# Optimization experiments

Measured on AMD Instinct MI355X. Metric: run time of the kernel, lower is better.

Reference implementation:

```python
import jax, jax.numpy as jnp
import numpy as np

B, T, D_MODEL = 2, 1024, 512
EXPAND = 2
D_INNER = D_MODEL * EXPAND
STATE = 16
K_CONV = 4


def setup_inputs() -> dict:
    key = jax.random.key(0)
    ks = jax.random.split(key, 10)
    sc = lambda k, shape: jax.random.normal(k, shape, jnp.float32) * 0.02
    return {
        "x": jax.random.normal(ks[0], (B, T, D_MODEL), jnp.float32),
        "ln_g": jnp.ones((D_MODEL,), jnp.float32),
        "ln_b": jnp.zeros((D_MODEL,), jnp.float32),
        "W_in": sc(ks[1], (2 * D_INNER, D_MODEL)),
        "conv_w": sc(ks[2], (D_INNER, 1, K_CONV)),
        "conv_b": jnp.zeros((D_INNER,), jnp.float32),
        "W_B": sc(ks[3], (STATE, D_INNER)),
        "W_C": sc(ks[4], (STATE, D_INNER)),
        "W_dt": sc(ks[5], (D_INNER, D_INNER)),
        "b_dt": jax.random.uniform(ks[6], (D_INNER,), jnp.float32, -4.0, -1.0),
        # log_A init: A_diag = -(n+1) from HiPPO, log(-A_diag) = log(n+1), broadcast over d_inner
        "log_A": jnp.broadcast_to(jnp.log(jnp.arange(1, STATE + 1, dtype=jnp.float32)), (D_INNER, STATE)),
        "W_out": sc(ks[7], (D_MODEL, D_INNER)),
    }


def _silu(v):
    return v * jax.nn.sigmoid(v)


def reference(x, ln_g, ln_b, W_in, conv_w, conv_b, W_B, W_C, W_dt, b_dt, log_A, W_out):
    residual = x
    # LayerNorm (biased variance, eps=1e-5)
    mu = x.mean(-1, keepdims=True)
    var = x.var(-1, keepdims=True)
    xn = (x - mu) * jax.lax.rsqrt(var + 1e-5) * ln_g + ln_b
    # input projection and gate split
    xz = xn @ W_in.T                      # (B,T,2*D_INNER)
    x_main, z = jnp.split(xz, 2, axis=-1)
    # depthwise causal conv1d (padding=3 then slice to T == left-pad 3)
    xc = jnp.transpose(x_main, (0, 2, 1))  # (B,D_INNER,T)
    xc = jax.lax.conv_general_dilated(
        xc, conv_w, window_strides=(1,), padding=[(K_CONV - 1, 0)],
        dimension_numbers=("NCH", "OIH", "NCH"), feature_group_count=D_INNER,
    ) + conv_b[None, :, None]
    x_main = _silu(jnp.transpose(xc, (0, 2, 1)))  # (B,T,D_INNER)
    # selective scan in fp32
    xf = x_main.astype(jnp.float32)
    Bt = xf @ W_B.T                        # (B,T,N)
    Ct = xf @ W_C.T                        # (B,T,N)
    dt = jax.nn.softplus(xf @ W_dt.T + b_dt)  # (B,T,D_INNER)
    A = -jnp.exp(log_A)                    # (D_INNER,N)
    dA = jnp.exp(A[None, None] * dt[..., None])              # (B,T,D_INNER,N)
    dBx = dt[..., None] * Bt[:, :, None, :] * xf[..., None]  # (B,T,D_INNER,N)

    def comb(c1, c2):
        a1, b1 = c1
        a2, b2 = c2
        return a1 * a2, a2 * b1 + b2

    _, h = jax.lax.associative_scan(comb, (dA, dBx), axis=1)  # h_t = dA_t*h_{t-1}+dBx_t
    y = (h * Ct[:, :, None, :]).sum(-1).astype(x.dtype)       # (B,T,D_INNER)
    out = (y * _silu(z)) @ W_out.T
    return residual + out
```

## Files before the change

### kernel.cpp

```cpp
#include <hip/hip_runtime.h>

#define T_SEQ 1024
#define DM 512
#define DI 1024
#define NS 16
#define NC 64
#define CL 16

typedef __attribute__((ext_vector_type(8))) short short8;
typedef __attribute__((ext_vector_type(4))) float f32x4;
typedef unsigned short u16;
typedef unsigned int u32;

__device__ inline float b2f(u16 u) {
    unsigned v = ((unsigned)u) << 16;
    return __builtin_bit_cast(float, v);
}
__device__ inline u16 f2b(float f) {
    unsigned u = __builtin_bit_cast(unsigned, f);
    u += 0x7fff + ((u >> 16) & 1);
    return (u16)(u >> 16);
}

__device__ inline void g2l16(const u16* g, short* l) {
    __builtin_amdgcn_global_load_lds((const __attribute__((address_space(1))) u32*)g,
                                     (__attribute__((address_space(3))) u32*)l, 16, 0, 0);
}

__global__ __launch_bounds__(256) void prep_k(const float* __restrict__ Win, const float* __restrict__ Wdt,
                       const float* __restrict__ Wout, const float* __restrict__ Wb,
                       const float* __restrict__ Wc,
                       u16* __restrict__ oWin, u16* __restrict__ oWdt, u16* __restrict__ oWout,
                       u16* __restrict__ oWb, u16* __restrict__ oWc,
                       const float* __restrict__ x, const float* __restrict__ g,
                       const float* __restrict__ be, u16* __restrict__ xn) {
    if (blockIdx.x < 2592) {
        int i = blockIdx.x * 256 + threadIdx.x;
        const float* s; u16* d; int off;
        if (i < 262144)      { s = Win;  d = oWin;  off = i; }
        else if (i < 524288) { s = Wdt;  d = oWdt;  off = i - 262144; }
        else if (i < 655360) { s = Wout; d = oWout; off = i - 524288; }
        else if (i < 659456) { s = Wb;   d = oWb;   off = i - 655360; }
        else                 { s = Wc;   d = oWc;   off = i - 659456; }
        float4 v = ((const float4*)s)[off];
        d[off * 4 + 0] = f2b(v.x);
        d[off * 4 + 1] = f2b(v.y);
        d[off * 4 + 2] = f2b(v.z);
        d[off * 4 + 3] = f2b(v.w);
        return;
    }
    int row = blockIdx.x - 2592, tid = threadIdx.x;
    float2 v = ((const float2*)(x + row * DM))[tid];
    float s = v.x + v.y, q = v.x * v.x + v.y * v.y;
    #pragma unroll
    for (int m = 1; m < 64; m <<= 1) { s += __shfl_xor(s, m); q += __shfl_xor(q, m); }
    __shared__ float ss[4], qq[4];
    if ((tid & 63) == 0) { ss[tid >> 6] = s; qq[tid >> 6] = q; }
    __syncthreads();
    s = ss[0] + ss[1] + ss[2] + ss[3];
    q = qq[0] + qq[1] + qq[2] + qq[3];
    float mu = s / DM;
    float var = q / DM - mu * mu;
    float rs = rsqrtf(var + 1e-5f);
    int c = tid * 2;
    xn[row * DM + c]     = f2b((v.x - mu) * rs * g[c] + be[c]);
    xn[row * DM + c + 1] = f2b((v.y - mu) * rs * g[c + 1] + be[c + 1]);
}

template<int BM, int BN, int NT, int EPI>
__global__ __launch_bounds__(256) void gemm_bt(const u16* __restrict__ A, int lda,
                                               const u16* __restrict__ Bw, int ldb,
                                               void* __restrict__ outp, int ldo,
                                               const float* __restrict__ extra) {
    __shared__ short a_sh[2][BM * 64];
    __shared__ short b_sh[2][BN * 64];
    constexpr int MI = BM / 32, NJ = BN / 32;
    int tid = threadIdx.x, w = tid >> 6, lane = tid & 63;
    int m0 = blockIdx.x * BM, n0 = blockIdx.y * BN;
    int wr = (w >> 1) * (BM / 2), wc = (w & 1) * (BN / 2);
    int lr = lane & 15, kg = lane >> 4;
    f32x4 acc[MI][NJ] = {};
    const u16* Abase = A + (size_t)m0 * lda;
    const u16* Bbase = Bw + (size_t)n0 * ldb;
    int lrow = lane >> 3;
    int lchunk = lane & 7;
    int schunk = lchunk ^ lrow;

    auto stage = [&](int cur, int kt) {
        int k0 = kt * 64;
        #pragma unroll
        for (int r = 0; r < BM / 32; ++r) {
            int row = r * 32 + w * 8 + lrow;
            g2l16(Abase + (size_t)row * lda + k0 + schunk * 8,
                  &a_sh[cur][(r * 32 + w * 8) * 64 + lane * 8]);
        }
        #pragma unroll
        for (int r = 0; r < BN / 32; ++r) {
            int row = r * 32 + w * 8 + lrow;
            g2l16(Bbase + (size_t)row * ldb + k0 + schunk * 8,
                  &b_sh[cur][(r * 32 + w * 8) * 64 + lane * 8]);
        }
    };

    stage(0, 0);
    __syncthreads();
    int cur = 0;
    for (int t = 0; t < NT; ++t) {
        if (t + 1 < NT) stage(cur ^ 1, t + 1);
        #pragma unroll
        for (int kk = 0; kk < 2; ++kk) {
            short8 af[MI], bfr[NJ];
            #pragma unroll
            for (int i = 0; i < MI; ++i) {
                int row = wr + i * 16 + lr;
                af[i] = *(const short8*)&a_sh[cur][row * 64 + (((kk << 2) | kg) ^ (row & 7)) * 8];
            }
            #pragma unroll
            for (int j = 0; j < NJ; ++j) {
                int row = wc + j * 16 + lr;
                bfr[j] = *(const short8*)&b_sh[cur][row * 64 + (((kk << 2) | kg) ^ (row & 7)) * 8];
            }
            #pragma unroll
            for (int i = 0; i < MI; ++i)
                #pragma unroll
                for (int j = 0; j < NJ; ++j)
                    acc[i][j] = __builtin_amdgcn_mfma_f32_16x16x32_bf16(af[i], bfr[j], acc[i][j], 0, 0, 0);
        }
        __syncthreads();
        cur ^= 1;
    }

    int rb = (lane >> 4) * 4, cc = lane & 15;
    #pragma unroll
    for (int i = 0; i < MI; ++i) {
        #pragma unroll
        for (int j = 0; j < NJ; ++j) {
            #pragma unroll
            for (int r = 0; r < 4; ++r) {
                int row = m0 + wr + i * 16 + rb + r;
                int col = n0 + wc + j * 16 + cc;
                float v = acc[i][j][r];
                if (EPI == 0) {
                    ((u16*)outp)[(size_t)row * ldo + col] = f2b(v);
                } else if (EPI == 1) {
                    float xx = v + extra[col];
                    float sp = (xx > 20.f) ? xx : log1pf(__expf(xx));
                    ((u16*)outp)[(size_t)row * ldo + col] = f2b(sp);
                } else {
                    ((float*)outp)[(size_t)row * ldo + col] = v + extra[(size_t)row * ldo + col];
                }
            }
        }
    }
}

__global__ void conv_k(const u16* __restrict__ xz, const float* __restrict__ w,
                       const float* __restrict__ cb, u16* __restrict__ xf) {
    int idx = blockIdx.x * 256 + threadIdx.x;
    int d = idx & (DI - 1);
    int bt = idx >> 10;
    int t = bt & (T_SEQ - 1);
    float s = cb[d];
    #pragma unroll
    for (int i = 0; i < 4; ++i) {
        int tt = t - 3 + i;
        if (tt >= 0) s += w[d * 4 + i] * b2f(xz[(size_t)(bt - 3 + i) * 2048 + d]);
    }
    float sig = 1.f / (1.f + __expf(-s));
    xf[idx] = f2b(s * sig);
}

__global__ __launch_bounds__(256) void bc_k(const u16* __restrict__ xf, const u16* __restrict__ Wb,
                                            const u16* __restrict__ Wc,
                                            float* __restrict__ Bt, float* __restrict__ Ct) {
    int m = blockIdx.x * 8 + (threadIdx.x >> 5);
    int j = threadIdx.x & 31;
    const u16* wrow = (j < 16) ? (Wb + j * DI) : (Wc + (j - 16) * DI);
    const short8* xr = (const short8*)(xf + (size_t)m * DI);
    const short8* wr = (const short8*)wrow;
    float s = 0.f;
    #pragma unroll 4
    for (int k = 0; k < DI / 8; ++k) {
        short8 a = xr[k], b = wr[k];
        #pragma unroll
        for (int e = 0; e < 8; ++e) s += b2f((u16)a[e]) * b2f((u16)b[e]);
    }
    float* o = (j < 16) ? Bt : Ct;
    o[(size_t)m * NS + (j & 15)] = s;
}

__global__ __launch_bounds__(256) void scanA(const u16* __restrict__ dt, const u16* __restrict__ xf,
                                             const float* __restrict__ Bt, const float* __restrict__ logA,
                                             float* __restrict__ Aprod, float* __restrict__ S) {
    int tid = threadIdx.x;
    int dblk = blockIdx.x & 3;
    int c = (blockIdx.x >> 2) & (NC - 1);
    int b = blockIdx.x >> 8;
    int d = dblk * 256 + tid;
    float Adn[NS], ap[NS], h[NS];
    #pragma unroll
    for (int j = 0; j < 4; ++j)
        *(float4*)&Adn[j * 4] = ((const float4*)(logA + (size_t)d * NS))[j];
    #pragma unroll
    for (int n = 0; n < NS; ++n) { Adn[n] = -__expf(Adn[n]); ap[n] = 1.f; h[n] = 0.f; }
    const u16* dtp = dt + ((size_t)b * T_SEQ + c * CL) * DI + d;
    const u16* xfp = xf + ((size_t)b * T_SEQ + c * CL) * DI + d;
    const float* Bp = Bt + ((size_t)b * T_SEQ + c * CL) * NS;
    #pragma unroll
    for (int i = 0; i < CL; ++i) {
        float dtv = b2f(dtp[(size_t)i * DI]);
        float xv  = b2f(xfp[(size_t)i * DI]);
        float ux = dtv * xv;
        float Bv[NS];
        #pragma unroll
        for (int j = 0; j < 4; ++j) *(float4*)&Bv[j * 4] = ((const float4*)(Bp + (size_t)i * NS))[j];
        #pragma unroll
        for (int n = 0; n < NS; ++n) {
            float dA = __expf(Adn[n] * dtv);
            h[n] = fmaf(dA, h[n], ux * Bv[n]);
            ap[n] *= dA;
        }
    }
    size_t o = ((((size_t)c * 2 + b) * DI) + d) * NS;
    #pragma unroll
    for (int j = 0; j < 4; ++j) {
        ((float4*)(Aprod + o))[j] = *(float4*)&ap[j * 4];
        ((float4*)(S + o))[j]     = *(float4*)&h[j * 4];
    }
}

__global__ __launch_bounds__(256) void scanB(const float* __restrict__ Aprod, const float* __restrict__ S,
                                             float* __restrict__ Hin) {
    int chain = blockIdx.x * 256 + threadIdx.x;
    float h = 0.f;
    #pragma unroll 8
    for (int c = 0; c < NC; ++c) {
        size_t o = (size_t)c * 32768 + chain;
        Hin[o] = h;
        h = fmaf(Aprod[o], h, S[o]);
    }
}

__global__ __launch_bounds__(256) void scanC(const u16* __restrict__ dt, const u16* __restrict__ xf,
                                             const float* __restrict__ Bt, const float* __restrict__ Ct,
                                             const float* __restrict__ logA, const float* __restrict__ Hin,
                                             const u16* __restrict__ xz, u16* __restrict__ ym) {
    int tid = threadIdx.x;
    int dblk = blockIdx.x & 3;
    int c = (blockIdx.x >> 2) & (NC - 1);
    int b = blockIdx.x >> 8;
    int d = dblk * 256 + tid;
    float Adn[NS], h[NS];
    #pragma unroll
    for (int j = 0; j < 4; ++j)
        *(float4*)&Adn[j * 4] = ((const float4*)(logA + (size_t)d * NS))[j];
    #pragma unroll
    for (int n = 0; n < NS; ++n) Adn[n] = -__expf(Adn[n]);
    size_t o = ((((size_t)c * 2 + b) * DI) + d) * NS;
    #pragma unroll
    for (int j = 0; j < 4; ++j) *(float4*)&h[j * 4] = ((const float4*)(Hin + o))[j];
    const u16* dtp = dt + ((size_t)b * T_SEQ + c * CL) * DI + d;
    const u16* xfp = xf + ((size_t)b * T_SEQ + c * CL) * DI + d;
    const float* Bp = Bt + ((size_t)b * T_SEQ + c * CL) * NS;
    const float* Cp = Ct + ((size_t)b * T_SEQ + c * CL) * NS;
    const u16* zp = xz + ((size_t)b * T_SEQ + c * CL) * 2048 + 1024 + d;
    u16* yp = ym + ((size_t)b * T_SEQ + c * CL) * DI + d;
    #pragma unroll
    for (int i = 0; i < CL; ++i) {
        float dtv = b2f(dtp[(size_t)i * DI]);
        float xv  = b2f(xfp[(size_t)i * DI]);
        float ux = dtv * xv;
        float Bv[NS], Cv[NS];
        #pragma unroll
        for (int j = 0; j < 4; ++j) {
            *(float4*)&Bv[j * 4] = ((const float4*)(Bp + (size_t)i * NS))[j];
            *(float4*)&Cv[j * 4] = ((const float4*)(Cp + (size_t)i * NS))[j];
        }
        float r = 0.f;
        #pragma unroll
        for (int n = 0; n < NS; ++n) {
            float dA = __expf(Adn[n] * dtv);
            h[n] = fmaf(dA, h[n], ux * Bv[n]);
            r = fmaf(h[n], Cv[n], r);
        }
        float zv = b2f(zp[(size_t)i * 2048]);
        float sz = zv / (1.f + __expf(-zv));
        yp[(size_t)i * DI] = f2b(r * sz);
    }
}

extern "C" void kernel_launch(void* const* d_in, const int* in_sizes, int n_in,
                              void* d_out, int out_size, void* d_ws, size_t ws_size,
                              hipStream_t stream) {
    const float* x     = (const float*)d_in[0];
    const float* ln_g  = (const float*)d_in[1];
    const float* ln_b  = (const float*)d_in[2];
    const float* W_in  = (const float*)d_in[3];
    const float* conv_w= (const float*)d_in[4];
    const float* conv_b= (const float*)d_in[5];
    const float* W_B   = (const float*)d_in[6];
    const float* W_C   = (const float*)d_in[7];
    const float* W_dt  = (const float*)d_in[8];
    const float* b_dt  = (const float*)d_in[9];
    const float* log_A = (const float*)d_in[10];
    const float* W_out = (const float*)d_in[11];

    char* ws = (char*)d_ws;
    u16* wInB  = (u16*)(ws + 0);
    u16* wDtB  = (u16*)(ws + 2097152);
    u16* wOutB = (u16*)(ws + 4194304);
    u16* wBB   = (u16*)(ws + 5242880);
    u16* wCB   = (u16*)(ws + 5275648);
    u16* xnB   = (u16*)(ws + 5308416);
    u16* xzB   = (u16*)(ws + 7405568);
    u16* xfB   = (u16*)(ws + 15794176);
    u16* dtB   = (u16*)(ws + 19988480);
    float* BtF = (float*)(ws + 24182784);
    float* CtF = (float*)(ws + 24313856);
    u16* ymB   = (u16*)(ws + 24444928);
    float* ApF = (float*)(ws + 28639232);
    float* SF  = (float*)(ws + 37027840);
    float* HiF = (float*)(ws + 45416448);

    prep_k<<<4640, 256, 0, stream>>>(W_in, W_dt, W_out, W_B, W_C, wInB, wDtB, wOutB, wBB, wCB,
                                     x, ln_g, ln_b, xnB);
    gemm_bt<64, 64, 8, 0><<<dim3(32, 32), 256, 0, stream>>>(xnB, 512, wInB, 512, (void*)xzB, 2048, nullptr);
    conv_k<<<8192, 256, 0, stream>>>(xzB, conv_w, conv_b, xfB);
    gemm_bt<64, 64, 16, 1><<<dim3(32, 16), 256, 0, stream>>>(xfB, 1024, wDtB, 1024, (void*)dtB, 1024, b_dt);
    bc_k<<<256, 256, 0, stream>>>(xfB, wBB, wCB, BtF, CtF);
    scanA<<<512, 256, 0, stream>>>(dtB, xfB, BtF, log_A, ApF, SF);
    scanB<<<128, 256, 0, stream>>>(ApF, SF, HiF);
    scanC<<<512, 256, 0, stream>>>(dtB, xfB, BtF, CtF, log_A, HiF, xzB, ymB);
    gemm_bt<32, 64, 16, 2><<<dim3(64, 8), 256, 0, stream>>>(ymB, 1024, wOutB, 1024, d_out, 512, x);
}
```

Baseline: 126.7 us.

## Fuse B/C projections into dt GEMM, triple-buffer GEMM loads, halve scan chunks

```diff
diff --git a/kernel.cpp b/kernel.cpp
--- a/kernel.cpp
+++ b/kernel.cpp
@@ -4,8 +4,8 @@
 #define DM 512
 #define DI 1024
 #define NS 16
-#define NC 64
-#define CL 16
+#define NC 32
+#define CL 32
 
 typedef __attribute__((ext_vector_type(8))) short short8;
 typedef __attribute__((ext_vector_type(4))) float f32x4;
@@ -22,26 +22,36 @@
     return (u16)(u >> 16);
 }
 
-__device__ inline void g2l16(const u16* g, short* l) {
+__device__ inline void g2l16(const u16* g, const short* l) {
     __builtin_amdgcn_global_load_lds((const __attribute__((address_space(1))) u32*)g,
                                      (__attribute__((address_space(3))) u32*)l, 16, 0, 0);
+}
+
+template<int K> __device__ __forceinline__ void vmwait() {
+    if constexpr (K == 0) asm volatile("s_waitcnt vmcnt(0)" ::: "memory");
+    else if constexpr (K == 3) asm volatile("s_waitcnt vmcnt(3)" ::: "memory");
+    else if constexpr (K == 4) asm volatile("s_waitcnt vmcnt(4)" ::: "memory");
 }
 
 __global__ __launch_bounds__(256) void prep_k(const float* __restrict__ Win, const float* __restrict__ Wdt,
                        const float* __restrict__ Wout, const float* __restrict__ Wb,
                        const float* __restrict__ Wc,
-                       u16* __restrict__ oWin, u16* __restrict__ oWdt, u16* __restrict__ oWout,
-                       u16* __restrict__ oWb, u16* __restrict__ oWc,
+                       u16* __restrict__ oWin, u16* __restrict__ wCat, u16* __restrict__ oWout,
                        const float* __restrict__ x, const float* __restrict__ g,
                        const float* __restrict__ be, u16* __restrict__ xn) {
-    if (blockIdx.x < 2592) {
+    if (blockIdx.x < 2624) {
         int i = blockIdx.x * 256 + threadIdx.x;
         const float* s; u16* d; int off;
         if (i < 262144)      { s = Win;  d = oWin;  off = i; }
-        else if (i < 524288) { s = Wdt;  d = oWdt;  off = i - 262144; }
+        else if (i < 524288) { s = Wdt;  d = wCat;  off = i - 262144; }
         else if (i < 655360) { s = Wout; d = oWout; off = i - 524288; }
-        else if (i < 659456) { s = Wb;   d = oWb;   off = i - 655360; }
-        else                 { s = Wc;   d = oWc;   off = i - 659456; }
+        else if (i < 659456) { s = Wb;   d = wCat + 1048576; off = i - 655360; }
+        else if (i < 663552) { s = Wc;   d = wCat + 1064960; off = i - 659456; }
+        else {
+            u16* dz = wCat + 1081344 + (i - 663552) * 4;
+            dz[0] = 0; dz[1] = 0; dz[2] = 0; dz[3] = 0;
+            return;
+        }
         float4 v = ((const float4*)s)[off];
         d[off * 4 + 0] = f2b(v.x);
         d[off * 4 + 1] = f2b(v.y);
@@ -49,7 +59,7 @@
         d[off * 4 + 3] = f2b(v.w);
         return;
     }
-    int row = blockIdx.x - 2592, tid = threadIdx.x;
+    int row = blockIdx.x - 2624, tid = threadIdx.x;
     float2 v = ((const float2*)(x + row * DM))[tid];
     float s = v.x + v.y, q = v.x * v.x + v.y * v.y;
     #pragma unroll
@@ -71,10 +81,14 @@
 __global__ __launch_bounds__(256) void gemm_bt(const u16* __restrict__ A, int lda,
                                                const u16* __restrict__ Bw, int ldb,
                                                void* __restrict__ outp, int ldo,
-                                               const float* __restrict__ extra) {
-    __shared__ short a_sh[2][BM * 64];
-    __shared__ short b_sh[2][BN * 64];
+                                               const float* __restrict__ extra,
+                                               float* __restrict__ BtF, float* __restrict__ CtF) {
+    constexpr int ASZ = BM * 64;
+    constexpr int BSZ = BN * 64;
+    constexpr int S = (BM + BN) / 32;
     constexpr int MI = BM / 32, NJ = BN / 32;
+    __shared__ short a_sh[3 * ASZ];
+    __shared__ short b_sh[3 * BSZ];
     int tid = threadIdx.x, w = tid >> 6, lane = tid & 63;
     int m0 = blockIdx.x * BM, n0 = blockIdx.y * BN;
     int wr = (w >> 1) * (BM / 2), wc = (w & 1) * (BN / 2);
@@ -82,43 +96,49 @@
     f32x4 acc[MI][NJ] = {};
     const u16* Abase = A + (size_t)m0 * lda;
     const u16* Bbase = Bw + (size_t)n0 * ldb;
-    int lrow = lane >> 3;
-    int lchunk = lane & 7;
-    int schunk = lchunk ^ lrow;
-
-    auto stage = [&](int cur, int kt) {
+    int lrow8 = lane >> 3;
+    int cl = lane & 7;
+
+    auto stage = [&](int buf, int kt) {
         int k0 = kt * 64;
         #pragma unroll
-        for (int r = 0; r < BM / 32; ++r) {
-            int row = r * 32 + w * 8 + lrow;
-            g2l16(Abase + (size_t)row * lda + k0 + schunk * 8,
-                  &a_sh[cur][(r * 32 + w * 8) * 64 + lane * 8]);
-        }
-        #pragma unroll
-        for (int r = 0; r < BN / 32; ++r) {
-            int row = r * 32 + w * 8 + lrow;
-            g2l16(Bbase + (size_t)row * ldb + k0 + schunk * 8,
-                  &b_sh[cur][(r * 32 + w * 8) * 64 + lane * 8]);
+        for (int q = 0; q < BM / 32; ++q) {
+            int rowbase = w * (BM / 4) + q * 8;
+            int row = rowbase + lrow8;
+            int sc = cl ^ lrow8;
+            g2l16(Abase + (size_t)row * lda + k0 + sc * 8, a_sh + buf * ASZ + rowbase * 64);
+        }
+        #pragma unroll
+        for (int q = 0; q < BN / 32; ++q) {
+            int rowbase = w * (BN / 4) + q * 8;
+            int row = rowbase + lrow8;
+            int sc = cl ^ lrow8;
+            g2l16(Bbase + (size_t)row * ldb + k0 + sc * 8, b_sh + buf * BSZ + rowbase * 64);
         }
     };
 
     stage(0, 0);
-    __syncthreads();
-    int cur = 0;
+    stage(1, 1);
     for (int t = 0; t < NT; ++t) {
-        if (t + 1 < NT) stage(cur ^ 1, t + 1);
+        if (t + 1 < NT) vmwait<S>();
+        else vmwait<0>();
+        asm volatile("s_barrier" ::: "memory");
+        if (t + 2 < NT) stage((t + 2) % 3, t + 2);
+        const short* as = a_sh + (t % 3) * ASZ;
+        const short* bs = b_sh + (t % 3) * BSZ;
+        int rs = lr & 7;
         #pragma unroll
         for (int kk = 0; kk < 2; ++kk) {
             short8 af[MI], bfr[NJ];
             #pragma unroll
             for (int i = 0; i < MI; ++i) {
                 int row = wr + i * 16 + lr;
-                af[i] = *(const short8*)&a_sh[cur][row * 64 + (((kk << 2) | kg) ^ (row & 7)) * 8];
+                af[i] = *(const short8*)&as[row * 64 + ((kk * 4 + kg) ^ rs) * 8];
             }
             #pragma unroll
             for (int j = 0; j < NJ; ++j) {
                 int row = wc + j * 16 + lr;
-                bfr[j] = *(const short8*)&b_sh[cur][row * 64 + (((kk << 2) | kg) ^ (row & 7)) * 8];
+                bfr[j] = *(const short8*)&bs[row * 64 + ((kk * 4 + kg) ^ rs) * 8];
             }
             #pragma unroll
             for (int i = 0; i < MI; ++i)
@@ -126,8 +146,6 @@
                 for (int j = 0; j < NJ; ++j)
                     acc[i][j] = __builtin_amdgcn_mfma_f32_16x16x32_bf16(af[i], bfr[j], acc[i][j], 0, 0, 0);
         }
-        __syncthreads();
-        cur ^= 1;
     }
 
     int rb = (lane >> 4) * 4, cc = lane & 15;
@@ -142,12 +160,18 @@
                 float v = acc[i][j][r];
                 if (EPI == 0) {
                     ((u16*)outp)[(size_t)row * ldo + col] = f2b(v);
-                } else if (EPI == 1) {
-                    float xx = v + extra[col];
-                    float sp = (xx > 20.f) ? xx : log1pf(__expf(xx));
-                    ((u16*)outp)[(size_t)row * ldo + col] = f2b(sp);
+                } else if (EPI == 2) {
+                    ((float*)outp)[(size_t)row * ldo + col] = v + extra[(size_t)row * ldo + col];
                 } else {
-                    ((float*)outp)[(size_t)row * ldo + col] = v + extra[(size_t)row * ldo + col];
+                    if (col < 1024) {
+                        float xx = v + extra[col];
+                        float sp = (xx > 20.f) ? xx : log1pf(__expf(xx));
+                        ((u16*)outp)[(size_t)row * ldo + col] = f2b(sp);
+                    } else if (col < 1040) {
+                        BtF[(size_t)row * NS + (col - 1024)] = v;
+                    } else if (col < 1056) {
+                        CtF[(size_t)row * NS + (col - 1040)] = v;
+                    }
                 }
             }
         }
@@ -170,32 +194,13 @@
     xf[idx] = f2b(s * sig);
 }
 
-__global__ __launch_bounds__(256) void bc_k(const u16* __restrict__ xf, const u16* __restrict__ Wb,
-                                            const u16* __restrict__ Wc,
-                                            float* __restrict__ Bt, float* __restrict__ Ct) {
-    int m = blockIdx.x * 8 + (threadIdx.x >> 5);
-    int j = threadIdx.x & 31;
-    const u16* wrow = (j < 16) ? (Wb + j * DI) : (Wc + (j - 16) * DI);
-    const short8* xr = (const short8*)(xf + (size_t)m * DI);
-    const short8* wr = (const short8*)wrow;
-    float s = 0.f;
-    #pragma unroll 4
-    for (int k = 0; k < DI / 8; ++k) {
-        short8 a = xr[k], b = wr[k];
-        #pragma unroll
-        for (int e = 0; e < 8; ++e) s += b2f((u16)a[e]) * b2f((u16)b[e]);
-    }
-    float* o = (j < 16) ? Bt : Ct;
-    o[(size_t)m * NS + (j & 15)] = s;
-}
-
 __global__ __launch_bounds__(256) void scanA(const u16* __restrict__ dt, const u16* __restrict__ xf,
                                              const float* __restrict__ Bt, const float* __restrict__ logA,
                                              float* __restrict__ Aprod, float* __restrict__ S) {
     int tid = threadIdx.x;
     int dblk = blockIdx.x & 3;
     int c = (blockIdx.x >> 2) & (NC - 1);
-    int b = blockIdx.x >> 8;
+    int b = blockIdx.x >> 7;
     int d = dblk * 256 + tid;
     float Adn[NS], ap[NS], h[NS];
     #pragma unroll
@@ -206,7 +211,7 @@
     const u16* dtp = dt + ((size_t)b * T_SEQ + c * CL) * DI + d;
     const u16* xfp = xf + ((size_t)b * T_SEQ + c * CL) * DI + d;
     const float* Bp = Bt + ((size_t)b * T_SEQ + c * CL) * NS;
-    #pragma unroll
+    #pragma unroll 8
     for (int i = 0; i < CL; ++i) {
         float dtv = b2f(dtp[(size_t)i * DI]);
         float xv  = b2f(xfp[(size_t)i * DI]);
@@ -248,7 +253,7 @@
     int tid = threadIdx.x;
     int dblk = blockIdx.x & 3;
     int c = (blockIdx.x >> 2) & (NC - 1);
-    int b = blockIdx.x >> 8;
+    int b = blockIdx.x >> 7;
     int d = dblk * 256 + tid;
     float Adn[NS], h[NS];
     #pragma unroll
@@ -265,7 +270,7 @@
     const float* Cp = Ct + ((size_t)b * T_SEQ + c * CL) * NS;
     const u16* zp = xz + ((size_t)b * T_SEQ + c * CL) * 2048 + 1024 + d;
     u16* yp = ym + ((size_t)b * T_SEQ + c * CL) * DI + d;
-    #pragma unroll
+    #pragma unroll 8
     for (int i = 0; i < CL; ++i) {
         float dtv = b2f(dtp[(size_t)i * DI]);
         float xv  = b2f(xfp[(size_t)i * DI]);
@@ -307,29 +312,29 @@
 
     char* ws = (char*)d_ws;
     u16* wInB  = (u16*)(ws + 0);
-    u16* wDtB  = (u16*)(ws + 2097152);
-    u16* wOutB = (u16*)(ws + 4194304);
-    u16* wBB   = (u16*)(ws + 5242880);
-    u16* wCB   = (u16*)(ws + 5275648);
-    u16* xnB   = (u16*)(ws + 5308416);
-    u16* xzB   = (u16*)(ws + 7405568);
-    u16* xfB   = (u16*)(ws + 15794176);
-    u16* dtB   = (u16*)(ws + 19988480);
-    float* BtF = (float*)(ws + 24182784);
-    float* CtF = (float*)(ws + 24313856);
-    u16* ymB   = (u16*)(ws + 24444928);
-    float* ApF = (float*)(ws + 28639232);
-    float* SF  = (float*)(ws + 37027840);
-    float* HiF = (float*)(ws + 45416448);
-
-    prep_k<<<4640, 256, 0, stream>>>(W_in, W_dt, W_out, W_B, W_C, wInB, wDtB, wOutB, wBB, wCB,
+    u16* wCat  = (u16*)(ws + 2097152);
+    u16* wOutB = (u16*)(ws + 4325376);
+    u16* xnB   = (u16*)(ws + 5373952);
+    u16* xzB   = (u16*)(ws + 7471104);
+    u16* xfB   = (u16*)(ws + 15859712);
+    u16* dtB   = (u16*)(ws + 20054016);
+    float* BtF = (float*)(ws + 24248320);
+    float* CtF = (float*)(ws + 24379392);
+    u16* ymB   = (u16*)(ws + 24510464);
+    float* ApF = (float*)(ws + 28704768);
+    float* SF  = (float*)(ws + 32899072);
+    float* HiF = (float*)(ws + 37093376);
+
+    prep_k<<<4672, 256, 0, stream>>>(W_in, W_dt, W_out, W_B, W_C, wInB, wCat, wOutB,
                                      x, ln_g, ln_b, xnB);
-    gemm_bt<64, 64, 8, 0><<<dim3(32, 32), 256, 0, stream>>>(xnB, 512, wInB, 512, (void*)xzB, 2048, nullptr);
+    gemm_bt<64, 64, 8, 0><<<dim3(32, 32), 256, 0, stream>>>(xnB, 512, wInB, 512,
+            (void*)xzB, 2048, nullptr, nullptr, nullptr);
     conv_k<<<8192, 256, 0, stream>>>(xzB, conv_w, conv_b, xfB);
-    gemm_bt<64, 64, 16, 1><<<dim3(32, 16), 256, 0, stream>>>(xfB, 1024, wDtB, 1024, (void*)dtB, 1024, b_dt);
-    bc_k<<<256, 256, 0, stream>>>(xfB, wBB, wCB, BtF, CtF);
-    scanA<<<512, 256, 0, stream>>>(dtB, xfB, BtF, log_A, ApF, SF);
+    gemm_bt<64, 64, 16, 4><<<dim3(32, 17), 256, 0, stream>>>(xfB, 1024, wCat, 1024,
+            (void*)dtB, 1024, b_dt, BtF, CtF);
+    scanA<<<256, 256, 0, stream>>>(dtB, xfB, BtF, log_A, ApF, SF);
     scanB<<<128, 256, 0, stream>>>(ApF, SF, HiF);
-    scanC<<<512, 256, 0, stream>>>(dtB, xfB, BtF, CtF, log_A, HiF, xzB, ymB);
-    gemm_bt<32, 64, 16, 2><<<dim3(64, 8), 256, 0, stream>>>(ymB, 1024, wOutB, 1024, d_out, 512, x);
-}
+    scanC<<<256, 256, 0, stream>>>(dtB, xfB, BtF, CtF, log_A, HiF, xzB, ymB);
+    gemm_bt<32, 64, 16, 2><<<dim3(64, 8), 256, 0, stream>>>(ymB, 1024, wOutB, 1024,
+            d_out, 512, x, nullptr, nullptr);
+}
```

After: 120.6 us. 4.8% less time.
